# Performance work log

Hardware: AMD Instinct MI355X
Metric: run time of the kernel (lower is better)

## Reference

```python
import jax, jax.numpy as jnp
import numpy as np

B, NV, NC, D, GD = 4, 2048, 8192, 64, 8


def setup_inputs() -> dict:
    key = jax.random.key(0)
    ks = jax.random.split(key, 16)
    f32 = jnp.float32
    rn = lambda k, s, fan: (jax.random.normal(k, s, dtype=f32) / np.float32(np.sqrt(fan)))
    raw = jax.random.randint(ks[0], (B, NC, NV), 0, 20)
    c_mat = jnp.where(raw == 0, -1.0, jnp.where(raw == 1, 1.0, 0.0)).astype(f32)
    v_mat = jnp.transpose(c_mat, (0, 2, 1))  # [B, NV, NC]
    variables = jax.random.normal(ks[1], (B, NV, D), dtype=f32)
    ground_vars = jax.random.normal(ks[2], (B, NV, GD), dtype=f32)
    # learned params
    c_block = rn(ks[3], (2, D, D), D)  # pos/neg literal projections (clause side)
    v_block = rn(ks[4], (2, D, D), D)  # pos/neg literal projections (variable side)
    vb = jax.random.normal(ks[5], (D,), dtype=f32)
    cb = jax.random.normal(ks[6], (D,), dtype=f32)
    Wg = rn(ks[7], (D, GD + D), GD + D)  # ground combiner Linear(concat) -> D
    bg = jnp.zeros((D,), f32)
    Wz = rn(ks[8], (D, D), D); Uz = rn(ks[9], (D, D), D); bz = jnp.zeros((D,), f32)
    Wr = rn(ks[10], (D, D), D); Ur = rn(ks[11], (D, D), D); br = jnp.zeros((D,), f32)
    Wh = rn(ks[12], (D, D), D); Uh = rn(ks[13], (D, D), D); bh = jnp.zeros((D,), f32)
    return dict(variables=variables, ground_vars=ground_vars, c_mat=c_mat, v_mat=v_mat,
                c_block=c_block, v_block=v_block, vb=vb, cb=cb, Wg=Wg, bg=bg,
                Wz=Wz, Uz=Uz, bz=bz, Wr=Wr, Ur=Ur, br=br, Wh=Wh, Uh=Uh, bh=bh)


def reference(variables, ground_vars, c_mat, v_mat, c_block, v_block, vb, cb,
              Wg, bg, Wz, Uz, bz, Wr, Ur, br, Wh, Uh, bh):
    b, nv, d = variables.shape
    v = variables.reshape(-1, d)  # [B*NV, D]
    # clause-side literal projections: bmm(c_block, v^T)^T == v @ c_block[i]^T
    pos_vars = (v @ c_block[0].T).reshape(b, nv, d)
    neg_vars = (v @ c_block[1].T).reshape(b, nv, d)
    pos_cmat = jnp.clip(c_mat, 0.0, 1.0)
    neg_cmat = -jnp.clip(c_mat, -1.0, 0.0)
    c = (jnp.einsum('bcv,bvd->bcd', pos_cmat, pos_vars)
         + jnp.einsum('bcv,bvd->bcd', neg_cmat, neg_vars))  # [B, NC, D]
    c = jax.nn.relu(c + cb)
    cv = c.reshape(-1, d)  # [B*NC, D]
    pos_cvars = (cv @ v_block[0].T).reshape(b, -1, d)
    neg_cvars = (cv @ v_block[1].T).reshape(b, -1, d)
    pos_vmat = jnp.clip(v_mat, 0.0, 1.0)
    neg_vmat = -jnp.clip(v_mat, -1.0, 0.0)
    nv_msg = (jnp.einsum('bvc,bcd->bvd', pos_vmat, pos_cvars)
              + jnp.einsum('bvc,bcd->bvd', neg_vmat, neg_cvars))  # [B, NV, D]
    v_emb = jax.nn.relu(nv_msg + vb).reshape(-1, d)
    # ground combiner: tanh(Linear(concat(ground, v_emb)))
    g = ground_vars.reshape(-1, ground_vars.shape[-1])
    av = jnp.tanh(jnp.concatenate([g, v_emb], axis=-1) @ Wg.T + bg)
    # GRU update against previous variable embeddings
    prev = v
    z = jax.nn.sigmoid(av @ Wz.T + prev @ Uz.T + bz)
    r = jax.nn.sigmoid(av @ Wr.T + prev @ Ur.T + br)
    h_tilda = jnp.tanh(av @ Wh.T + (r * prev) @ Uh.T + bh)
    h = (1.0 - z) * prev + z * h_tilda
    return h.reshape(b, nv * d, 1)
```

## Files before the change

### kernel.cpp

```cpp
#include <hip/hip_runtime.h>
#include <hip/hip_bf16.h>
#include <stdint.h>

#define NBATCH 4
#define NV 2048
#define NC 8192
#define DD 64

typedef __attribute__((ext_vector_type(8))) short s16x8;
typedef __attribute__((ext_vector_type(4))) float fx4;
typedef __attribute__((ext_vector_type(8))) unsigned short u16x8;
typedef __attribute__((ext_vector_type(4))) int i32x4;
typedef __attribute__((ext_vector_type(2))) unsigned int u32x2;

static __device__ __forceinline__ void gload_lds16(const void* g, void* l) {
    __builtin_amdgcn_global_load_lds(
        (const __attribute__((address_space(1))) unsigned int*)g,
        (__attribute__((address_space(3))) unsigned int*)l, 16, 0, 0);
}

__global__ __launch_bounds__(256) void k_prep_pv(
    const float* __restrict__ vars, const float* __restrict__ cblk,
    char* __restrict__ qsh, char* __restrict__ qsl,
    char* __restrict__ qdh, char* __restrict__ qdl)
{
    __shared__ float sv[32][64];
    __shared__ float scb[2][64][65];
    int blk = blockIdx.x;
    int b = blk >> 6, ch = blk & 63;
    int t = threadIdx.x;
    const float* vsrc = vars + ((size_t)b * NV + (size_t)ch * 32) * DD;
    for (int i = t; i < 32 * 64; i += 256) sv[i >> 6][i & 63] = vsrc[i];
    for (int i = t; i < 2 * 64 * 64; i += 256) {
        int pn = i >> 12, dout = (i >> 6) & 63, k = i & 63;
        scb[pn][k][dout] = cblk[i];
    }
    __syncthreads();
    int ks = t >> 6, dout = t & 63;
    unsigned int wsh[2] = {0, 0}, wsl[2] = {0, 0}, wdh[2] = {0, 0}, wdl[2] = {0, 0};
    #pragma unroll
    for (int c8 = 0; c8 < 8; ++c8) {
        int vloc = ks * 8 + c8;
        float ap = 0.f, an = 0.f;
        for (int k = 0; k < 64; ++k) {
            float vv = sv[vloc][k];
            ap += vv * scb[0][k][dout];
            an += vv * scb[1][k][dout];
        }
        float s = (ap + an) * 0.5f, dv = (ap - an) * 0.5f;
        int qs_ = (int)rintf(s * 4096.f);
        int qd_ = (int)rintf(dv * 4096.f);
        qs_ = min(max(qs_, -32511), 32511);
        qd_ = min(max(qd_, -32511), 32511);
        int sh = (qs_ + 128) >> 8, sl = qs_ - (sh << 8);
        int dh = (qd_ + 128) >> 8, dl = qd_ - (dh << 8);
        int w = c8 >> 2, sft = (c8 & 3) * 8;
        wsh[w] |= (unsigned int)(sh & 0xFF) << sft;
        wsl[w] |= (unsigned int)(sl & 0xFF) << sft;
        wdh[w] |= (unsigned int)(dh & 0xFF) << sft;
        wdl[w] |= (unsigned int)(dl & 0xFF) << sft;
    }
    int kc = ch >> 1;
    int lg = ((ch & 1) << 1) | (ks >> 1);
    size_t off = (((size_t)(b * 32 + kc) * 64 + dout) * 4 + lg) * 16 + (ks & 1) * 8;
    *(u32x2*)(qsh + off) = (u32x2){wsh[0], wsh[1]};
    *(u32x2*)(qsl + off) = (u32x2){wsl[0], wsl[1]};
    *(u32x2*)(qdh + off) = (u32x2){wdh[0], wdh[1]};
    *(u32x2*)(qdl + off) = (u32x2){wdl[0], wdl[1]};
}

__global__ __launch_bounds__(256, 2) void k_phaseA(
    const float* __restrict__ cmat,
    const char* __restrict__ qsh, const char* __restrict__ qsl,
    const char* __restrict__ qdh, const char* __restrict__ qdl,
    float* __restrict__ cpart, unsigned short* __restrict__ comp)
{
    __shared__ char lds[2][16384];
    int blk = blockIdx.x;
    int combo = blk & 15;
    int rg = blk >> 4;
    int b = combo >> 2;
    int q = combo & 3;
    int t = threadIdx.x;
    int wv = t >> 6, l = t & 63, lr = l & 15, lg = l >> 4;
    int c0 = rg * 128 + wv * 32;
    const float* A0 = cmat + (size_t)b * NC * NV + (size_t)lr * NV + q * 512 + lg * 16;
    unsigned short* compb = comp + (size_t)b * 256 * NC;

    i32x4 ahi[2][4], alo[2][4];
    #pragma unroll
    for (int i = 0; i < 2; ++i)
        #pragma unroll
        for (int j = 0; j < 4; ++j) { ahi[i][j] = (i32x4){0,0,0,0}; alo[i][j] = (i32x4){0,0,0,0}; }

    {
        size_t gb = ((size_t)(b * 32 + q * 8)) * 4096 + (size_t)t * 16;
        char* lp = &lds[0][t * 16];
        gload_lds16(qsh + gb, lp);
        gload_lds16(qsl + gb, lp + 4096);
        gload_lds16(qdh + gb, lp + 8192);
        gload_lds16(qdl + gb, lp + 12288);
    }
    fx4 xc[2][4], xn[2][4];
    #pragma unroll
    for (int rt = 0; rt < 2; ++rt)
        #pragma unroll
        for (int j4 = 0; j4 < 4; ++j4)
            xc[rt][j4] = *(const fx4*)(A0 + (size_t)(c0 + rt * 16) * NV + j4 * 4);
    __syncthreads();

    int cur = 0;
    #pragma unroll 1
    for (int cc = 0; cc < 8; ++cc) {
        if (cc < 7) {
            size_t gb = ((size_t)(b * 32 + q * 8 + cc + 1)) * 4096 + (size_t)t * 16;
            char* lp = &lds[cur ^ 1][t * 16];
            gload_lds16(qsh + gb, lp);
            gload_lds16(qsl + gb, lp + 4096);
            gload_lds16(qdh + gb, lp + 8192);
            gload_lds16(qdl + gb, lp + 12288);
            #pragma unroll
            for (int rt = 0; rt < 2; ++rt)
                #pragma unroll
                for (int j4 = 0; j4 < 4; ++j4)
                    xn[rt][j4] = *(const fx4*)(A0 + (size_t)(c0 + rt * 16) * NV + (cc + 1) * 64 + j4 * 4);
        }
        i32x4 Asgn[2], Aabs[2];
        #pragma unroll
        for (int rt = 0; rt < 2; ++rt) {
            int tt[16];
            #pragma unroll
            for (int j = 0; j < 16; ++j) tt[j] = (int)xc[rt][j >> 2][j & 3];
            i32x4 sg;
            #pragma unroll
            for (int w = 0; w < 4; ++w)
                sg[w] = (unsigned int)(tt[4*w] & 0xFF) | ((unsigned int)(tt[4*w+1] & 0xFF) << 8)
                      | ((unsigned int)(tt[4*w+2] & 0xFF) << 16) | ((unsigned int)(tt[4*w+3] & 0xFF) << 24);
            Asgn[rt] = sg;
            i32x4 ab;
            #pragma unroll
            for (int w = 0; w < 4; ++w) ab[w] = sg[w] & 0x01010101;
            Aabs[rt] = ab;
            unsigned int b0 = 0, b1 = 0;
            #pragma unroll
            for (int j = 0; j < 8; ++j) b0 |= ((unsigned int)tt[j] & 3u) << (2 * j);
            #pragma unroll
            for (int j = 0; j < 8; ++j) b1 |= ((unsigned int)tt[8 + j] & 3u) << (2 * j);
            int v8 = q * 64 + cc * 8 + lg * 2;
            int crow = c0 + rt * 16 + lr;
            compb[(size_t)v8 * NC + crow] = (unsigned short)b0;
            compb[(size_t)(v8 + 1) * NC + crow] = (unsigned short)b1;
        }
        const char* bufp = lds[cur];
        #pragma unroll
        for (int n = 0; n < 4; ++n) {
            int boff = ((n * 16 + lr) * 4 + lg) * 16;
            i32x4 Bsh = *(const i32x4*)(bufp + boff);
            i32x4 Bsl = *(const i32x4*)(bufp + 4096 + boff);
            i32x4 Bdh = *(const i32x4*)(bufp + 8192 + boff);
            i32x4 Bdl = *(const i32x4*)(bufp + 12288 + boff);
            #pragma unroll
            for (int rt = 0; rt < 2; ++rt) {
                ahi[rt][n] = __builtin_amdgcn_mfma_i32_16x16x64_i8(Aabs[rt], Bsh, ahi[rt][n], 0, 0, 0);
                ahi[rt][n] = __builtin_amdgcn_mfma_i32_16x16x64_i8(Asgn[rt], Bdh, ahi[rt][n], 0, 0, 0);
                alo[rt][n] = __builtin_amdgcn_mfma_i32_16x16x64_i8(Aabs[rt], Bsl, alo[rt][n], 0, 0, 0);
                alo[rt][n] = __builtin_amdgcn_mfma_i32_16x16x64_i8(Asgn[rt], Bdl, alo[rt][n], 0, 0, 0);
            }
        }
        if (cc < 7) {
            #pragma unroll
            for (int rt = 0; rt < 2; ++rt)
                #pragma unroll
                for (int j4 = 0; j4 < 4; ++j4) xc[rt][j4] = xn[rt][j4];
        }
        __syncthreads();
        cur ^= 1;
    }
    float* dst = cpart + (((size_t)q * NBATCH + b) * NC + c0) * DD;
    #pragma unroll
    for (int rt = 0; rt < 2; ++rt)
        #pragma unroll
        for (int n = 0; n < 4; ++n)
            #pragma unroll
            for (int r = 0; r < 4; ++r) {
                float v = (float)(ahi[rt][n][r] * 256 + alo[rt][n][r]) * (1.0f / 4096.0f);
                dst[(size_t)(rt * 16 + lg * 4 + r) * DD + n * 16 + lr] = v;
            }
}

__global__ __launch_bounds__(256) void k_projC(
    const float* __restrict__ cpart, const float* __restrict__ cb,
    const float* __restrict__ vblk,
    char* __restrict__ csh, char* __restrict__ csl,
    char* __restrict__ cdh, char* __restrict__ cdl)
{
    __shared__ float src[32][64];
    __shared__ float svb[2][64][65];
    int blk = blockIdx.x;
    int b = blk >> 8, kc32 = blk & 255;
    int t = threadIdx.x;
    const size_t qs = (size_t)NBATCH * NC * DD;
    const float* cs = cpart + ((size_t)b * NC + (size_t)kc32 * 32) * DD;
    for (int i = t; i < 2048; i += 256) {
        int k = i & 63;
        float v = cb[k];
        #pragma unroll
        for (int p = 0; p < 4; ++p) v += cs[i + p * qs];
        src[i >> 6][k] = fmaxf(v, 0.f);
    }
    for (int i = t; i < 8192; i += 256) {
        int pn = i >> 12, dout = (i >> 6) & 63, k = i & 63;
        svb[pn][k][dout] = vblk[i];
    }
    __syncthreads();
    int ks = t >> 6, dout = t & 63;
    float ap[8] = {0.f, 0.f, 0.f, 0.f, 0.f, 0.f, 0.f, 0.f};
    float an[8] = {0.f, 0.f, 0.f, 0.f, 0.f, 0.f, 0.f, 0.f};
    for (int k = 0; k < 64; ++k) {
        float w0 = svb[0][k][dout], w1 = svb[1][k][dout];
        #pragma unroll
        for (int c8 = 0; c8 < 8; ++c8) {
            float rc = src[ks * 8 + c8][k];
            ap[c8] += rc * w0;
            an[c8] += rc * w1;
        }
    }
    unsigned int wsh[2] = {0, 0}, wsl[2] = {0, 0}, wdh[2] = {0, 0}, wdl[2] = {0, 0};
    #pragma unroll
    for (int c8 = 0; c8 < 8; ++c8) {
        float s = (ap[c8] + an[c8]) * 0.5f, dv = (ap[c8] - an[c8]) * 0.5f;
        int q_s = (int)rintf(s * 512.f);
        int q_d = (int)rintf(dv * 512.f);
        q_s = min(max(q_s, -32511), 32511);
        q_d = min(max(q_d, -32511), 32511);
        int sh = (q_s + 128) >> 8, sl = q_s - (sh << 8);
        int dh = (q_d + 128) >> 8, dl = q_d - (dh << 8);
        int w = c8 >> 2, sft = (c8 & 3) * 8;
        wsh[w] |= (unsigned int)(sh & 0xFF) << sft;
        wsl[w] |= (unsigned int)(sl & 0xFF) << sft;
        wdh[w] |= (unsigned int)(dh & 0xFF) << sft;
        wdl[w] |= (unsigned int)(dl & 0xFF) << sft;
    }
    int kc = kc32 >> 1;
    int lgw = ((kc32 & 1) << 1) | (ks >> 1);
    size_t off = (((size_t)(b * 128 + kc) * 64 + dout) * 4 + lgw) * 16 + (ks & 1) * 8;
    *(u32x2*)(csh + off) = (u32x2){wsh[0], wsh[1]};
    *(u32x2*)(csl + off) = (u32x2){wsl[0], wsl[1]};
    *(u32x2*)(cdh + off) = (u32x2){wdh[0], wdh[1]};
    *(u32x2*)(cdl + off) = (u32x2){wdl[0], wdl[1]};
}

__global__ __launch_bounds__(256, 4) void k_phaseB(
    const unsigned short* __restrict__ comp,
    const char* __restrict__ csh, const char* __restrict__ csl,
    const char* __restrict__ cdh, const char* __restrict__ cdl,
    float* __restrict__ npart)
{
    __shared__ char lds[2][16384];
    int blk = blockIdx.x;
    int combo = blk & 63;
    int rg = blk >> 6;
    int b = combo >> 4;
    int q = combo & 15;
    int t = threadIdx.x;
    int wv = t >> 6, l = t & 63, lr = l & 15, lg = l >> 4;
    int v0 = rg * 128 + wv * 32;
    const unsigned short* compb = comp + (size_t)b * 256 * NC;
    int sh_ = 2 * (lr & 7);
    const unsigned short* cp0 = compb + (size_t)((v0 + lr) >> 3) * NC + q * 512 + lg * 16;
    const unsigned short* cp1 = compb + (size_t)((v0 + 16 + lr) >> 3) * NC + q * 512 + lg * 16;
    const size_t cbase = ((size_t)(b * 128 + q * 8)) * 4096;

    i32x4 ahi[2][4], alo[2][4];
    #pragma unroll
    for (int i = 0; i < 2; ++i)
        #pragma unroll
        for (int j = 0; j < 4; ++j) { ahi[i][j] = (i32x4){0,0,0,0}; alo[i][j] = (i32x4){0,0,0,0}; }

    {
        size_t gb = cbase + (size_t)t * 16;
        char* lp = &lds[0][t * 16];
        gload_lds16(csh + gb, lp);
        gload_lds16(csl + gb, lp + 4096);
        gload_lds16(cdh + gb, lp + 8192);
        gload_lds16(cdl + gb, lp + 12288);
    }
    __syncthreads();

    int cur = 0;
    #pragma unroll 1
    for (int cc = 0; cc < 8; ++cc) {
        u16x8 u00 = *(const u16x8*)(cp0 + cc * 64);
        u16x8 u01 = *(const u16x8*)(cp0 + cc * 64 + 8);
        u16x8 u10 = *(const u16x8*)(cp1 + cc * 64);
        u16x8 u11 = *(const u16x8*)(cp1 + cc * 64 + 8);
        if (cc < 7) {
            size_t gb = cbase + (size_t)(cc + 1) * 4096 + (size_t)t * 16;
            char* lp = &lds[cur ^ 1][t * 16];
            gload_lds16(csh + gb, lp);
            gload_lds16(csl + gb, lp + 4096);
            gload_lds16(cdh + gb, lp + 8192);
            gload_lds16(cdl + gb, lp + 12288);
        }
        i32x4 Asgn[2], Aabs[2];
        #pragma unroll
        for (int rt = 0; rt < 2; ++rt) {
            u16x8 ua = rt ? u10 : u00;
            u16x8 ub = rt ? u11 : u01;
            i32x4 sg;
            #pragma unroll
            for (int g = 0; g < 4; ++g) {
                unsigned int wg = 0;
                #pragma unroll
                for (int jj = 0; jj < 4; ++jj) {
                    int j = g * 4 + jj;
                    unsigned int code = ((unsigned int)(j < 8 ? ua[j & 7] : ub[j & 7]) >> sh_) & 3u;
                    unsigned int byt = (code == 3u) ? 0xFFu : code;
                    wg |= byt << (jj * 8);
                }
                sg[g] = (int)wg;
            }
            Asgn[rt] = sg;
            i32x4 ab;
            #pragma unroll
            for (int g = 0; g < 4; ++g) ab[g] = sg[g] & 0x01010101;
            Aabs[rt] = ab;
        }
        const char* bufp = lds[cur];
        #pragma unroll
        for (int n = 0; n < 4; ++n) {
            int boff = ((n * 16 + lr) * 4 + lg) * 16;
            i32x4 Bsh = *(const i32x4*)(bufp + boff);
            i32x4 Bsl = *(const i32x4*)(bufp + 4096 + boff);
            i32x4 Bdh = *(const i32x4*)(bufp + 8192 + boff);
            i32x4 Bdl = *(const i32x4*)(bufp + 12288 + boff);
            #pragma unroll
            for (int rt = 0; rt < 2; ++rt) {
                ahi[rt][n] = __builtin_amdgcn_mfma_i32_16x16x64_i8(Aabs[rt], Bsh, ahi[rt][n], 0, 0, 0);
                ahi[rt][n] = __builtin_amdgcn_mfma_i32_16x16x64_i8(Asgn[rt], Bdh, ahi[rt][n], 0, 0, 0);
                alo[rt][n] = __builtin_amdgcn_mfma_i32_16x16x64_i8(Aabs[rt], Bsl, alo[rt][n], 0, 0, 0);
                alo[rt][n] = __builtin_amdgcn_mfma_i32_16x16x64_i8(Asgn[rt], Bdl, alo[rt][n], 0, 0, 0);
            }
        }
        __syncthreads();
        cur ^= 1;
    }
    float* dst = npart + (((size_t)q * NBATCH + b) * NV + v0) * DD;
    #pragma unroll
    for (int rt = 0; rt < 2; ++rt)
        #pragma unroll
        for (int n = 0; n < 4; ++n)
            #pragma unroll
            for (int r = 0; r < 4; ++r) {
                float v = (float)(ahi[rt][n][r] * 256 + alo[rt][n][r]) * (1.0f / 512.0f);
                dst[(size_t)(rt * 16 + lg * 4 + r) * DD + n * 16 + lr] = v;
            }
}

__global__ __launch_bounds__(512) void k_gru(
    const float* __restrict__ npart, const float* __restrict__ vars,
    const float* __restrict__ gv, const float* __restrict__ vb,
    const float* __restrict__ Wg, const float* __restrict__ bg,
    const float* __restrict__ Wz, const float* __restrict__ Uz, const float* __restrict__ bz,
    const float* __restrict__ Wr, const float* __restrict__ Ur, const float* __restrict__ brr,
    const float* __restrict__ Wh, const float* __restrict__ Uh, const float* __restrict__ bh,
    float* __restrict__ out)
{
    __shared__ float sWg[72][65];
    __shared__ float sWz[64][65], sUz[64][65];
    __shared__ float sWr[64][65], sUr[64][65];
    __shared__ float sWh[64][65], sUh[64][65];
    __shared__ float scat[8][72];
    __shared__ float sprev[8][64];
    __shared__ float sav[8][64];
    __shared__ float srp[8][64];
    int t = threadIdx.x;
    for (int i = t * 4; i < 4608; i += 2048) {
        fx4 g4 = *(const fx4*)(Wg + i);
        int dout = i / 72, j = i - dout * 72;
        #pragma unroll
        for (int jj = 0; jj < 4; ++jj) sWg[j + jj][dout] = g4[jj];
    }
    for (int i = t * 4; i < 4096; i += 2048) {
        int dout = i >> 6, k = i & 63;
        fx4 a;
        a = *(const fx4*)(Wz + i);
        #pragma unroll
        for (int jj = 0; jj < 4; ++jj) sWz[k + jj][dout] = a[jj];
        a = *(const fx4*)(Uz + i);
        #pragma unroll
        for (int jj = 0; jj < 4; ++jj) sUz[k + jj][dout] = a[jj];
        a = *(const fx4*)(Wr + i);
        #pragma unroll
        for (int jj = 0; jj < 4; ++jj) sWr[k + jj][dout] = a[jj];
        a = *(const fx4*)(Ur + i);
        #pragma unroll
        for (int jj = 0; jj < 4; ++jj) sUr[k + jj][dout] = a[jj];
        a = *(const fx4*)(Wh + i);
        #pragma unroll
        for (int jj = 0; jj < 4; ++jj) sWh[k + jj][dout] = a[jj];
        a = *(const fx4*)(Uh + i);
        #pragma unroll
        for (int jj = 0; jj < 4; ++jj) sUh[k + jj][dout] = a[jj];
    }
    int rr = t >> 6, dout = t & 63;
    const size_t qs = (size_t)NBATCH * NV * DD;
    #pragma unroll 1
    for (int it = 0; it < 4; ++it) {
        size_t row = (size_t)blockIdx.x * 32 + it * 8 + rr;
        float prev = vars[row * 64 + dout];
        float ve = vb[dout];
        #pragma unroll
        for (int s = 0; s < 16; ++s) ve += npart[(size_t)s * qs + row * 64 + dout];
        ve = fmaxf(ve, 0.f);
        scat[rr][8 + dout] = ve;
        if (dout < 8) scat[rr][dout] = gv[row * 8 + dout];
        sprev[rr][dout] = prev;
        __syncthreads();
        float a = bg[dout];
        for (int j = 0; j < 72; ++j) a += scat[rr][j] * sWg[j][dout];
        float av = 1.f - 2.f / (__expf(2.f * a) + 1.f);
        sav[rr][dout] = av;
        __syncthreads();
        float zi = bz[dout], ri = brr[dout], hwa = 0.f;
        for (int k = 0; k < 64; ++k) {
            float ak = sav[rr][k], pk = sprev[rr][k];
            zi += ak * sWz[k][dout] + pk * sUz[k][dout];
            ri += ak * sWr[k][dout] + pk * sUr[k][dout];
            hwa += ak * sWh[k][dout];
        }
        float z = 1.f / (1.f + __expf(-zi));
        float rgate = 1.f / (1.f + __expf(-ri));
        srp[rr][dout] = rgate * prev;
        __syncthreads();
        float hin = bh[dout] + hwa;
        for (int k = 0; k < 64; ++k) hin += srp[rr][k] * sUh[k][dout];
        float ht = 1.f - 2.f / (__expf(2.f * hin) + 1.f);
        out[row * 64 + dout] = (1.f - z) * prev + z * ht;
        __syncthreads();
    }
}

extern "C" void kernel_launch(void* const* d_in, const int* in_sizes, int n_in,
                              void* d_out, int out_size, void* d_ws, size_t ws_size,
                              hipStream_t stream) {
    (void)in_sizes; (void)n_in; (void)out_size; (void)ws_size;
    const float* vars = (const float*)d_in[0];
    const float* gv   = (const float*)d_in[1];
    const float* cmat = (const float*)d_in[2];
    const float* cblk = (const float*)d_in[4];
    const float* vblk = (const float*)d_in[5];
    const float* vb   = (const float*)d_in[6];
    const float* cb   = (const float*)d_in[7];
    const float* Wg   = (const float*)d_in[8];
    const float* bg   = (const float*)d_in[9];
    const float* Wz   = (const float*)d_in[10];
    const float* Uz   = (const float*)d_in[11];
    const float* bz   = (const float*)d_in[12];
    const float* Wr   = (const float*)d_in[13];
    const float* Ur   = (const float*)d_in[14];
    const float* br_  = (const float*)d_in[15];
    const float* Wh   = (const float*)d_in[16];
    const float* Uh   = (const float*)d_in[17];
    const float* bh   = (const float*)d_in[18];
    float* out = (float*)d_out;

    char* w = (char*)d_ws;
    const size_t MB = 1024 * 1024;
    char* qsh = w + 0 * MB;
    char* qsl = w + 1 * MB;
    char* qdh = w + 2 * MB;
    char* qdl = w + 3 * MB;
    char* csh = w + 4 * MB;
    char* csl = w + 6 * MB;
    char* cdh = w + 8 * MB;
    char* cdl = w + 10 * MB;
    float* cpart         = (float*)(w + 12 * MB);
    float* npart         = (float*)(w + 44 * MB);
    unsigned short* comp = (unsigned short*)(w + 76 * MB);

    k_prep_pv<<<256, 256, 0, stream>>>(vars, cblk, qsh, qsl, qdh, qdl);
    k_phaseA<<<1024, 256, 0, stream>>>(cmat, qsh, qsl, qdh, qdl, cpart, comp);
    k_projC<<<1024, 256, 0, stream>>>(cpart, cb, vblk, csh, csl, cdh, cdl);
    k_phaseB<<<1024, 256, 0, stream>>>(comp, csh, csl, cdh, cdl, npart);
    k_gru<<<256, 512, 0, stream>>>(npart, vars, gv, vb, Wg, bg,
                                   Wz, Uz, bz, Wr, Ur, br_, Wh, Uh, bh, out);
}
```

Baseline: 165.4 us.

## Split c_mat compression into separate kernel feeding int8 operands to phaseA

Moves the float-to-int8 packing of c_mat and the 2-bit compressed adjacency generation out of the MFMA kernel into a dedicated k_compress kernel that stages rows through LDS and writes coalesced int8 tiles. phaseA then reads the prepacked 64 MB-smaller int8 operand instead of fp32 rows, with launch bounds raised to allow more occupancy. It adds an extra kernel launch and an intermediate 64 MB int8 buffer round trip, trading one large fused read for a read plus write plus reread.

```diff
diff --git a/kernel.cpp b/kernel.cpp
--- a/kernel.cpp
+++ b/kernel.cpp
@@ -69,11 +69,55 @@
     *(u32x2*)(qdl + off) = (u32x2){wdl[0], wdl[1]};
 }
 
-__global__ __launch_bounds__(256, 2) void k_phaseA(
+__global__ __launch_bounds__(256) void k_compress(
     const float* __restrict__ cmat,
+    char* __restrict__ asgn, unsigned short* __restrict__ comp)
+{
+    __shared__ char sb[64][272];
+    int blk = blockIdx.x;
+    int tv = blk & 7;
+    int rg = (blk >> 3) & 127;
+    int b = blk >> 10;
+    int t = threadIdx.x;
+    int wv = t >> 6, l = t & 63;
+    int crow0 = rg * 64;
+    const float* src = cmat + (size_t)b * NC * NV + (size_t)crow0 * NV + tv * 256;
+    #pragma unroll 4
+    for (int rr = 0; rr < 16; ++rr) {
+        int r = wv * 16 + rr;
+        fx4 x = *(const fx4*)(src + (size_t)r * NV + l * 4);
+        unsigned int pk = ((unsigned int)((int)x[0] & 0xFF))
+                        | (((unsigned int)((int)x[1] & 0xFF)) << 8)
+                        | (((unsigned int)((int)x[2] & 0xFF)) << 16)
+                        | (((unsigned int)((int)x[3] & 0xFF)) << 24);
+        *(unsigned int*)&sb[r][l * 4] = pk;
+    }
+    __syncthreads();
+    size_t abase = ((size_t)(b * 128 + tv * 16)) * 8192 * 16;
+    #pragma unroll
+    for (int ff = 0; ff < 4; ++ff) {
+        int f = wv * 4 + ff;
+        i32x4 v = *(const i32x4*)&sb[l][f * 16];
+        *(i32x4*)(asgn + abase + ((size_t)f * 8192 + crow0 + l) * 16) = v;
+    }
+    unsigned short* cbp = comp + ((size_t)b * 256 + tv * 32) * NC + crow0;
+    #pragma unroll
+    for (int it = 0; it < 8; ++it) {
+        int idx = it * 256 + t;
+        int v8l = idx >> 6, r = idx & 63;
+        const unsigned char* p = (const unsigned char*)&sb[r][v8l * 8];
+        unsigned int c0 = 0;
+        #pragma unroll
+        for (int i = 0; i < 8; ++i) c0 |= ((unsigned int)(p[i] & 3u)) << (2 * i);
+        cbp[(size_t)v8l * NC + r] = (unsigned short)c0;
+    }
+}
+
+__global__ __launch_bounds__(256, 4) void k_phaseA(
+    const char* __restrict__ asgn,
     const char* __restrict__ qsh, const char* __restrict__ qsl,
     const char* __restrict__ qdh, const char* __restrict__ qdl,
-    float* __restrict__ cpart, unsigned short* __restrict__ comp)
+    float* __restrict__ cpart)
 {
     __shared__ char lds[2][16384];
     int blk = blockIdx.x;
@@ -84,8 +128,6 @@
     int t = threadIdx.x;
     int wv = t >> 6, l = t & 63, lr = l & 15, lg = l >> 4;
     int c0 = rg * 128 + wv * 32;
-    const float* A0 = cmat + (size_t)b * NC * NV + (size_t)lr * NV + q * 512 + lg * 16;
-    unsigned short* compb = comp + (size_t)b * 256 * NC;
 
     i32x4 ahi[2][4], alo[2][4];
     #pragma unroll
@@ -101,55 +143,31 @@
         gload_lds16(qdh + gb, lp + 8192);
         gload_lds16(qdl + gb, lp + 12288);
     }
-    fx4 xc[2][4], xn[2][4];
-    #pragma unroll
-    for (int rt = 0; rt < 2; ++rt)
-        #pragma unroll
-        for (int j4 = 0; j4 < 4; ++j4)
-            xc[rt][j4] = *(const fx4*)(A0 + (size_t)(c0 + rt * 16) * NV + j4 * 4);
     __syncthreads();
 
     int cur = 0;
     #pragma unroll 1
     for (int cc = 0; cc < 8; ++cc) {
+        int kc = q * 8 + cc;
         if (cc < 7) {
-            size_t gb = ((size_t)(b * 32 + q * 8 + cc + 1)) * 4096 + (size_t)t * 16;
+            size_t gb = ((size_t)(b * 32 + kc + 1)) * 4096 + (size_t)t * 16;
             char* lp = &lds[cur ^ 1][t * 16];
             gload_lds16(qsh + gb, lp);
             gload_lds16(qsl + gb, lp + 4096);
             gload_lds16(qdh + gb, lp + 8192);
             gload_lds16(qdl + gb, lp + 12288);
-            #pragma unroll
-            for (int rt = 0; rt < 2; ++rt)
-                #pragma unroll
-                for (int j4 = 0; j4 < 4; ++j4)
-                    xn[rt][j4] = *(const fx4*)(A0 + (size_t)(c0 + rt * 16) * NV + (cc + 1) * 64 + j4 * 4);
         }
         i32x4 Asgn[2], Aabs[2];
         #pragma unroll
         for (int rt = 0; rt < 2; ++rt) {
-            int tt[16];
-            #pragma unroll
-            for (int j = 0; j < 16; ++j) tt[j] = (int)xc[rt][j >> 2][j & 3];
-            i32x4 sg;
-            #pragma unroll
-            for (int w = 0; w < 4; ++w)
-                sg[w] = (unsigned int)(tt[4*w] & 0xFF) | ((unsigned int)(tt[4*w+1] & 0xFF) << 8)
-                      | ((unsigned int)(tt[4*w+2] & 0xFF) << 16) | ((unsigned int)(tt[4*w+3] & 0xFF) << 24);
+            size_t ao = (((size_t)(b * 128 + kc * 4 + lg)) * 8192
+                         + (size_t)(c0 + rt * 16 + lr)) * 16;
+            i32x4 sg = *(const i32x4*)(asgn + ao);
             Asgn[rt] = sg;
             i32x4 ab;
             #pragma unroll
             for (int w = 0; w < 4; ++w) ab[w] = sg[w] & 0x01010101;
             Aabs[rt] = ab;
-            unsigned int b0 = 0, b1 = 0;
-            #pragma unroll
-            for (int j = 0; j < 8; ++j) b0 |= ((unsigned int)tt[j] & 3u) << (2 * j);
-            #pragma unroll
-            for (int j = 0; j < 8; ++j) b1 |= ((unsigned int)tt[8 + j] & 3u) << (2 * j);
-            int v8 = q * 64 + cc * 8 + lg * 2;
-            int crow = c0 + rt * 16 + lr;
-            compb[(size_t)v8 * NC + crow] = (unsigned short)b0;
-            compb[(size_t)(v8 + 1) * NC + crow] = (unsigned short)b1;
         }
         const char* bufp = lds[cur];
         #pragma unroll
@@ -166,12 +184,6 @@
                 alo[rt][n] = __builtin_amdgcn_mfma_i32_16x16x64_i8(Aabs[rt], Bsl, alo[rt][n], 0, 0, 0);
                 alo[rt][n] = __builtin_amdgcn_mfma_i32_16x16x64_i8(Asgn[rt], Bdl, alo[rt][n], 0, 0, 0);
             }
-        }
-        if (cc < 7) {
-            #pragma unroll
-            for (int rt = 0; rt < 2; ++rt)
-                #pragma unroll
-                for (int j4 = 0; j4 < 4; ++j4) xc[rt][j4] = xn[rt][j4];
         }
         __syncthreads();
         cur ^= 1;
@@ -478,9 +490,11 @@
     float* cpart         = (float*)(w + 12 * MB);
     float* npart         = (float*)(w + 44 * MB);
     unsigned short* comp = (unsigned short*)(w + 76 * MB);
+    char* asgn           = w + 92 * MB;
 
     k_prep_pv<<<256, 256, 0, stream>>>(vars, cblk, qsh, qsl, qdh, qdl);
-    k_phaseA<<<1024, 256, 0, stream>>>(cmat, qsh, qsl, qdh, qdl, cpart, comp);
+    k_compress<<<4096, 256, 0, stream>>>(cmat, asgn, comp);
+    k_phaseA<<<1024, 256, 0, stream>>>(asgn, qsh, qsl, qdh, qdl, cpart);
     k_projC<<<1024, 256, 0, stream>>>(cpart, cb, vblk, csh, csl, cdh, cdl);
     k_phaseB<<<1024, 256, 0, stream>>>(comp, csh, csl, cdh, cdl, npart);
     k_gru<<<256, 512, 0, stream>>>(npart, vars, gv, vb, Wg, bg,
```

After: 186.3 us. +12.6%, slower.
